# Performance work log

Hardware: AMD Instinct MI355X
Metric: run time of the kernel (lower is better)

The kernel has to match this reference:

```python
import jax, jax.numpy as jnp
import numpy as np

B, T, C = 4, 2048, 1024
H = 16
D = C // H  # 64


def setup_inputs() -> dict:
    key = jax.random.key(0)
    ks = jax.random.split(key, 3)
    scale = 1.0 / np.sqrt(C)
    return {
        "x": jax.random.normal(ks[0], (B, T, C), dtype=jnp.float32),
        "W_attn": jax.random.normal(ks[1], (C, 3 * C), dtype=jnp.float32) * scale,
        "b_attn": jnp.zeros((3 * C,), dtype=jnp.float32),
        "W_proj": jax.random.normal(ks[2], (C, C), dtype=jnp.float32) * scale,
        "b_proj": jnp.zeros((C,), dtype=jnp.float32),
    }


def reference(x, W_attn, b_attn, W_proj, b_proj):
    b, t, c = x.shape
    qkv = x @ W_attn + b_attn                      # [B,T,3C]
    q, k, v = jnp.split(qkv, 3, axis=-1)           # each [B,T,C]
    to_heads = lambda z: z.reshape(b, t, H, D).transpose(0, 2, 1, 3)  # [B,H,T,D]
    q, k, v = to_heads(q), to_heads(k), to_heads(v)
    scores = jnp.einsum("bhtd,bhsd->bhts", q, k) / jnp.sqrt(jnp.float32(D))
    causal = jnp.tril(jnp.ones((t, t), dtype=bool))  # [T,T]
    scores = jnp.where(causal[None, None], scores, jnp.finfo(scores.dtype).min)
    attn = jax.nn.softmax(scores, axis=-1)           # [B,H,T,T]
    out = jnp.einsum("bhts,bhsd->bhtd", attn, v)     # [B,H,T,D]
    out = out.transpose(0, 2, 1, 3).reshape(b, t, c)
    return out @ W_proj + b_proj
```

## Files before the change

### kernel.cpp

```cpp
#include <hip/hip_runtime.h>
#include <hip/hip_bf16.h>

typedef __bf16 bf16_t;
typedef __attribute__((ext_vector_type(8))) __bf16 bf16x8;
typedef __attribute__((ext_vector_type(4))) float f32x4;
typedef __attribute__((ext_vector_type(4))) unsigned short u16x4;

#define B_DIM 4
#define T_DIM 2048
#define C_DIM 1024
#define H_DIM 16
#define D_DIM 64
#define M_TOK (B_DIM * T_DIM)
#define N_QKV (3 * C_DIM)
#define NT    (T_DIM / 64)
#define KSTR  72
#define CSC   0.18033688011112042f

__device__ __forceinline__ void gload_lds16(const bf16_t* g, bf16_t* l) {
  __builtin_amdgcn_global_load_lds((const __attribute__((address_space(1))) void*)(g),
                                   (__attribute__((address_space(3))) void*)(l), 16, 0, 0);
}

__global__ void cvt_f32_to_bf16(const float* __restrict__ in, bf16_t* __restrict__ out, int n4) {
  int i = blockIdx.x * blockDim.x + threadIdx.x;
  if (i >= n4) return;
  float4 v = ((const float4*)in)[i];
  struct alignas(8) bv4 { bf16_t x, y, z, w; };
  bv4 o;
  o.x = (bf16_t)v.x; o.y = (bf16_t)v.y; o.z = (bf16_t)v.z; o.w = (bf16_t)v.w;
  ((bv4*)out)[i] = o;
}

__global__ void transpose_f32_to_bf16(const float* __restrict__ in, bf16_t* __restrict__ out,
                                      int K, int N) {
  __shared__ float tile[32][33];
  int bx = blockIdx.x * 32;
  int by = blockIdx.y * 32;
  int tx = threadIdx.x, ty = threadIdx.y;
#pragma unroll
  for (int i = 0; i < 32; i += 8)
    tile[ty + i][tx] = in[(size_t)(by + ty + i) * N + bx + tx];
  __syncthreads();
#pragma unroll
  for (int i = 0; i < 32; i += 8)
    out[(size_t)(bx + ty + i) * K + by + tx] = (bf16_t)tile[tx][ty + i];
}

#define BM 128
#define BN 128
#define BK 32

__global__ __launch_bounds__(256, 4)
void gemm_bt_bias(const bf16_t* __restrict__ A, const bf16_t* __restrict__ Bt,
                  const float* __restrict__ bias, bf16_t* __restrict__ Cb,
                  int M, int N, int K) {
  __shared__ alignas(16) bf16_t As[BM * BK];
  __shared__ alignas(16) bf16_t Bs[BN * BK];
  const int tid = threadIdx.x;
  const int lane = tid & 63;
  const int wave = tid >> 6;
  const int wr = (wave >> 1) * 64, wc = (wave & 1) * 64;
  const int quad = lane >> 4, l16 = lane & 15;
  const int row0 = blockIdx.x * BM, col0 = blockIdx.y * BN;

  const int srow = wave * 32 + (lane >> 2);
  const int scol = (lane & 3) * 8;
  const bf16_t* Ag = A + (size_t)(row0 + srow) * K + scol;
  const bf16_t* Bg = Bt + (size_t)(col0 + srow) * K + scol;
  bf16_t* AsW = &As[(wave * 32) * BK];
  bf16_t* BsW = &Bs[(wave * 32) * BK];

  f32x4 acc[4][4];
#pragma unroll
  for (int i = 0; i < 4; ++i)
#pragma unroll
    for (int j = 0; j < 4; ++j)
      acc[i][j] = (f32x4){0.f, 0.f, 0.f, 0.f};

  for (int k0 = 0; k0 < K; k0 += BK) {
    __syncthreads();
    gload_lds16(Ag + k0, AsW);
    gload_lds16(Ag + k0 + (size_t)16 * K, AsW + 16 * BK);
    gload_lds16(Bg + k0, BsW);
    gload_lds16(Bg + k0 + (size_t)16 * K, BsW + 16 * BK);
    __syncthreads();
    bf16x8 af[4], bfr[4];
#pragma unroll
    for (int i = 0; i < 4; ++i)
      af[i] = *(const bf16x8*)&As[(wr + i * 16 + l16) * BK + quad * 8];
#pragma unroll
    for (int j = 0; j < 4; ++j)
      bfr[j] = *(const bf16x8*)&Bs[(wc + j * 16 + l16) * BK + quad * 8];
#pragma unroll
    for (int i = 0; i < 4; ++i)
#pragma unroll
      for (int j = 0; j < 4; ++j)
        acc[i][j] = __builtin_amdgcn_mfma_f32_16x16x32_bf16(af[i], bfr[j], acc[i][j], 0, 0, 0);
  }

#pragma unroll
  for (int i = 0; i < 4; ++i)
#pragma unroll
    for (int j = 0; j < 4; ++j) {
      int col = col0 + wc + j * 16 + l16;
      float bv = bias[col];
#pragma unroll
      for (int r = 0; r < 4; ++r) {
        int row = row0 + wr + i * 16 + quad * 4 + r;
        Cb[(size_t)row * N + col] = (bf16_t)(acc[i][j][r] + bv);
      }
    }
}

__global__ __launch_bounds__(256, 4)
void gemm_bt_bias_n64(const bf16_t* __restrict__ A, const bf16_t* __restrict__ Bt,
                      const float* __restrict__ bias, float* __restrict__ Cf,
                      int M, int N, int K) {
  __shared__ alignas(16) bf16_t As[BM * BK];
  __shared__ alignas(16) bf16_t Bs[64 * BK];
  const int tid = threadIdx.x;
  const int lane = tid & 63;
  const int wave = tid >> 6;
  const int wr = (wave >> 1) * 64, wc = (wave & 1) * 32;
  const int quad = lane >> 4, l16 = lane & 15;
  const int row0 = blockIdx.x * BM, col0 = blockIdx.y * 64;

  const int sr = lane >> 2;
  const int scol = (lane & 3) * 8;
  const bf16_t* Ag = A + (size_t)(row0 + wave * 32 + sr) * K + scol;
  const bf16_t* Bg = Bt + (size_t)(col0 + wave * 16 + sr) * K + scol;
  bf16_t* AsW = &As[(wave * 32) * BK];
  bf16_t* BsW = &Bs[(wave * 16) * BK];

  f32x4 acc[4][2];
#pragma unroll
  for (int i = 0; i < 4; ++i)
#pragma unroll
    for (int j = 0; j < 2; ++j)
      acc[i][j] = (f32x4){0.f, 0.f, 0.f, 0.f};

  for (int k0 = 0; k0 < K; k0 += BK) {
    __syncthreads();
    gload_lds16(Ag + k0, AsW);
    gload_lds16(Ag + k0 + (size_t)16 * K, AsW + 16 * BK);
    gload_lds16(Bg + k0, BsW);
    __syncthreads();
    bf16x8 af[4], bfr[2];
#pragma unroll
    for (int i = 0; i < 4; ++i)
      af[i] = *(const bf16x8*)&As[(wr + i * 16 + l16) * BK + quad * 8];
#pragma unroll
    for (int j = 0; j < 2; ++j)
      bfr[j] = *(const bf16x8*)&Bs[(wc + j * 16 + l16) * BK + quad * 8];
#pragma unroll
    for (int i = 0; i < 4; ++i)
#pragma unroll
      for (int j = 0; j < 2; ++j)
        acc[i][j] = __builtin_amdgcn_mfma_f32_16x16x32_bf16(af[i], bfr[j], acc[i][j], 0, 0, 0);
  }

#pragma unroll
  for (int i = 0; i < 4; ++i)
#pragma unroll
    for (int j = 0; j < 2; ++j) {
      int col = col0 + wc + j * 16 + l16;
      float bv = bias[col];
#pragma unroll
      for (int r = 0; r < 4; ++r) {
        int row = row0 + wr + i * 16 + quad * 4 + r;
        Cf[(size_t)row * N + col] = acc[i][j][r] + bv;
      }
    }
}

__device__ __forceinline__ float exp_row_sum(f32x4 sv[4], bool diag, bf16_t* PsW,
                                             int l16, int quad, int wave) {
  if (diag) {
    const int qr = wave * 16 + l16;
#pragma unroll
    for (int ct = 0; ct < 4; ++ct)
#pragma unroll
      for (int r = 0; r < 4; ++r)
        if (ct * 16 + quad * 4 + r > qr) sv[ct][r] = -INFINITY;
  }
  float rsum = 0.f;
#pragma unroll
  for (int ct = 0; ct < 4; ++ct) {
    u16x4 pk;
#pragma unroll
    for (int r = 0; r < 4; ++r) {
      float p = __builtin_amdgcn_exp2f(sv[ct][r] * CSC);
      rsum += p;
      pk[r] = __builtin_bit_cast(unsigned short, (bf16_t)p);
    }
    *(u16x4*)&PsW[l16 * KSTR + ct * 16 + quad * 4] = pk;
  }
  rsum += __shfl_xor(rsum, 16);
  rsum += __shfl_xor(rsum, 32);
  return rsum;
}

__global__ __launch_bounds__(256, 4)
void attn_fwd(const bf16_t* __restrict__ qkv, bf16_t* __restrict__ out) {
  __shared__ alignas(16) bf16_t Ks[64 * KSTR];
  __shared__ alignas(16) bf16_t Vt[64 * KSTR];
  __shared__ alignas(16) bf16_t Ps[4 * 16 * KSTR];

  const int tid = threadIdx.x;
  const int lane = tid & 63;
  const int wave = tid >> 6;
  const int quad = lane >> 4, l16 = lane & 15;
  const int qlo = blockIdx.x;
  const int qhi = NT - 1 - qlo;
  const int h = blockIdx.y, b = blockIdx.z;
  const size_t tokBase = (size_t)b * T_DIM;

  const bf16_t* qpl = qkv + (tokBase + qlo * 64 + wave * 16 + l16) * N_QKV + h * D_DIM;
  const bf16_t* qph = qkv + (tokBase + qhi * 64 + wave * 16 + l16) * N_QKV + h * D_DIM;
  bf16x8 ql0 = *(const bf16x8*)(qpl + quad * 8);
  bf16x8 ql1 = *(const bf16x8*)(qpl + 32 + quad * 8);
  bf16x8 qh0 = *(const bf16x8*)(qph + quad * 8);
  bf16x8 qh1 = *(const bf16x8*)(qph + 32 + quad * 8);

  f32x4 ol[4], oh[4];
#pragma unroll
  for (int dt = 0; dt < 4; ++dt) {
    ol[dt] = (f32x4){0.f, 0.f, 0.f, 0.f};
    oh[dt] = (f32x4){0.f, 0.f, 0.f, 0.f};
  }
  float ll = 0.f, lh = 0.f;

  const int tx = tid & 15, ty = tid >> 4;
  bf16_t* PsW = &Ps[wave * 16 * KSTR];
  const f32x4 zero4 = (f32x4){0.f, 0.f, 0.f, 0.f};

  u16x4 kreg[4], vreg[4];
  const bf16_t* kb0 = qkv + (tokBase + ty * 4) * N_QKV + h * D_DIM + C_DIM + tx * 4;
#pragma unroll
  for (int r = 0; r < 4; ++r) kreg[r] = *(const u16x4*)(kb0 + (size_t)r * N_QKV);
#pragma unroll
  for (int r = 0; r < 4; ++r) vreg[r] = *(const u16x4*)(kb0 + (size_t)r * N_QKV + C_DIM);

  for (int t = 0; t <= qhi; ++t) {
    const bool lo = (t <= qlo);
    __syncthreads();
#pragma unroll
    for (int r = 0; r < 4; ++r)
      *(u16x4*)&Ks[(ty * 4 + r) * KSTR + tx * 4] = kreg[r];
#pragma unroll
    for (int i = 0; i < 4; ++i) {
      u16x4 p = (u16x4){vreg[0][i], vreg[1][i], vreg[2][i], vreg[3][i]};
      *(u16x4*)&Vt[(tx * 4 + i) * KSTR + ty * 4] = p;
    }
    __syncthreads();
    if (t < qhi) {
      const bf16_t* kb = qkv + (tokBase + (t + 1) * 64 + ty * 4) * N_QKV + h * D_DIM + C_DIM + tx * 4;
#pragma unroll
      for (int r = 0; r < 4; ++r) kreg[r] = *(const u16x4*)(kb + (size_t)r * N_QKV);
#pragma unroll
      for (int r = 0; r < 4; ++r) vreg[r] = *(const u16x4*)(kb + (size_t)r * N_QKV + C_DIM);
    }

    f32x4 svl[4], svh[4];
#pragma unroll
    for (int ct = 0; ct < 4; ++ct) {
      bf16x8 kf0 = *(const bf16x8*)&Ks[(ct * 16 + l16) * KSTR + quad * 8];
      bf16x8 kf1 = *(const bf16x8*)&Ks[(ct * 16 + l16) * KSTR + 32 + quad * 8];
      if (lo) {
        svl[ct] = __builtin_amdgcn_mfma_f32_16x16x32_bf16(kf0, ql0, zero4, 0, 0, 0);
        svl[ct] = __builtin_amdgcn_mfma_f32_16x16x32_bf16(kf1, ql1, svl[ct], 0, 0, 0);
      }
      svh[ct] = __builtin_amdgcn_mfma_f32_16x16x32_bf16(kf0, qh0, zero4, 0, 0, 0);
      svh[ct] = __builtin_amdgcn_mfma_f32_16x16x32_bf16(kf1, qh1, svh[ct], 0, 0, 0);
    }

    bf16x8 pl0, pl1, ph0, ph1;
    if (lo) {
      ll += exp_row_sum(svl, t == qlo, PsW, l16, quad, wave);
      pl0 = *(const bf16x8*)&PsW[l16 * KSTR + quad * 8];
      pl1 = *(const bf16x8*)&PsW[l16 * KSTR + 32 + quad * 8];
    }
    lh += exp_row_sum(svh, t == qhi, PsW, l16, quad, wave);
    ph0 = *(const bf16x8*)&PsW[l16 * KSTR + quad * 8];
    ph1 = *(const bf16x8*)&PsW[l16 * KSTR + 32 + quad * 8];

#pragma unroll
    for (int dt = 0; dt < 4; ++dt) {
      bf16x8 vf0 = *(const bf16x8*)&Vt[(dt * 16 + l16) * KSTR + quad * 8];
      bf16x8 vf1 = *(const bf16x8*)&Vt[(dt * 16 + l16) * KSTR + 32 + quad * 8];
      if (lo) {
        ol[dt] = __builtin_amdgcn_mfma_f32_16x16x32_bf16(vf0, pl0, ol[dt], 0, 0, 0);
        ol[dt] = __builtin_amdgcn_mfma_f32_16x16x32_bf16(vf1, pl1, ol[dt], 0, 0, 0);
      }
      oh[dt] = __builtin_amdgcn_mfma_f32_16x16x32_bf16(vf0, ph0, oh[dt], 0, 0, 0);
      oh[dt] = __builtin_amdgcn_mfma_f32_16x16x32_bf16(vf1, ph1, oh[dt], 0, 0, 0);
    }
  }

  struct alignas(8) bh4 { bf16_t a, b, c, d; };
  {
    float rl = 1.0f / ll;
    bf16_t* op = out + (tokBase + qlo * 64 + wave * 16 + l16) * C_DIM + h * D_DIM;
#pragma unroll
    for (int dt = 0; dt < 4; ++dt) {
      bh4 v = {(bf16_t)(ol[dt][0] * rl), (bf16_t)(ol[dt][1] * rl),
               (bf16_t)(ol[dt][2] * rl), (bf16_t)(ol[dt][3] * rl)};
      *(bh4*)(op + dt * 16 + quad * 4) = v;
    }
  }
  {
    float rl = 1.0f / lh;
    bf16_t* op = out + (tokBase + qhi * 64 + wave * 16 + l16) * C_DIM + h * D_DIM;
#pragma unroll
    for (int dt = 0; dt < 4; ++dt) {
      bh4 v = {(bf16_t)(oh[dt][0] * rl), (bf16_t)(oh[dt][1] * rl),
               (bf16_t)(oh[dt][2] * rl), (bf16_t)(oh[dt][3] * rl)};
      *(bh4*)(op + dt * 16 + quad * 4) = v;
    }
  }
}

extern "C" void kernel_launch(void* const* d_in, const int* in_sizes, int n_in,
                              void* d_out, int out_size, void* d_ws, size_t ws_size,
                              hipStream_t stream) {
  const float* x      = (const float*)d_in[0];
  const float* W_attn = (const float*)d_in[1];
  const float* b_attn = (const float*)d_in[2];
  const float* W_proj = (const float*)d_in[3];
  const float* b_proj = (const float*)d_in[4];
  float* out = (float*)d_out;

  char* ws = (char*)d_ws;
  bf16_t* xb   = (bf16_t*)ws;  ws += (size_t)M_TOK * C_DIM * 2;
  bf16_t* Wat  = (bf16_t*)ws;  ws += (size_t)N_QKV * C_DIM * 2;
  bf16_t* Wpt  = (bf16_t*)ws;  ws += (size_t)C_DIM * C_DIM * 2;
  bf16_t* qkv  = (bf16_t*)ws;  ws += (size_t)M_TOK * N_QKV * 2;
  bf16_t* attn = (bf16_t*)ws;  ws += (size_t)M_TOK * C_DIM * 2;

  {
    int n4 = (M_TOK * C_DIM) / 4;
    cvt_f32_to_bf16<<<n4 / 256, 256, 0, stream>>>(x, xb, n4);
  }
  transpose_f32_to_bf16<<<dim3(N_QKV / 32, C_DIM / 32), dim3(32, 8), 0, stream>>>(W_attn, Wat, C_DIM, N_QKV);
  transpose_f32_to_bf16<<<dim3(C_DIM / 32, C_DIM / 32), dim3(32, 8), 0, stream>>>(W_proj, Wpt, C_DIM, C_DIM);

  gemm_bt_bias<<<dim3(M_TOK / BM, N_QKV / BN), 256, 0, stream>>>(
      xb, Wat, b_attn, qkv, M_TOK, N_QKV, C_DIM);

  attn_fwd<<<dim3(NT / 2, H_DIM, B_DIM), 256, 0, stream>>>(qkv, attn);

  gemm_bt_bias_n64<<<dim3(M_TOK / BM, C_DIM / 64), 256, 0, stream>>>(
      attn, Wpt, b_proj, out, M_TOK, C_DIM, C_DIM);
}
```

Before: 280.8 us.

## Replace paired lo/hi query-tile attention blocks with one tile per block

The attention kernel no longer pairs a short causal tile with a long one in each block for load balance. Each block now handles a single 64-row query tile, the grid doubles, and blocks are ordered longest-first so heavy tiles start early. Each K/V tile loaded into LDS now feeds only one query tile instead of two, but each block needs fewer registers and a block's work ends at its own diagonal. Packed-integer types are also swapped for bf16 vector types, which is cosmetic.

```diff
diff --git a/kernel.cpp b/kernel.cpp
--- a/kernel.cpp
+++ b/kernel.cpp
@@ -2,9 +2,9 @@
 #include <hip/hip_bf16.h>
 
 typedef __bf16 bf16_t;
+typedef __attribute__((ext_vector_type(4))) __bf16 bf16x4;
 typedef __attribute__((ext_vector_type(8))) __bf16 bf16x8;
 typedef __attribute__((ext_vector_type(4))) float f32x4;
-typedef __attribute__((ext_vector_type(4))) unsigned short u16x4;
 
 #define B_DIM 4
 #define T_DIM 2048
@@ -26,10 +26,9 @@
   int i = blockIdx.x * blockDim.x + threadIdx.x;
   if (i >= n4) return;
   float4 v = ((const float4*)in)[i];
-  struct alignas(8) bv4 { bf16_t x, y, z, w; };
-  bv4 o;
-  o.x = (bf16_t)v.x; o.y = (bf16_t)v.y; o.z = (bf16_t)v.z; o.w = (bf16_t)v.w;
-  ((bv4*)out)[i] = o;
+  bf16x4 o;
+  o[0] = (bf16_t)v.x; o[1] = (bf16_t)v.y; o[2] = (bf16_t)v.z; o[3] = (bf16_t)v.w;
+  ((bf16x4*)out)[i] = o;
 }
 
 __global__ void transpose_f32_to_bf16(const float* __restrict__ in, bf16_t* __restrict__ out,
@@ -187,14 +186,14 @@
   float rsum = 0.f;
 #pragma unroll
   for (int ct = 0; ct < 4; ++ct) {
-    u16x4 pk;
+    bf16x4 pk;
 #pragma unroll
     for (int r = 0; r < 4; ++r) {
       float p = __builtin_amdgcn_exp2f(sv[ct][r] * CSC);
       rsum += p;
-      pk[r] = __builtin_bit_cast(unsigned short, (bf16_t)p);
-    }
-    *(u16x4*)&PsW[l16 * KSTR + ct * 16 + quad * 4] = pk;
+      pk[r] = (bf16_t)p;
+    }
+    *(bf16x4*)&PsW[l16 * KSTR + ct * 16 + quad * 4] = pk;
   }
   rsum += __shfl_xor(rsum, 16);
   rsum += __shfl_xor(rsum, 32);
@@ -211,113 +210,80 @@
   const int lane = tid & 63;
   const int wave = tid >> 6;
   const int quad = lane >> 4, l16 = lane & 15;
-  const int qlo = blockIdx.x;
-  const int qhi = NT - 1 - qlo;
+  const int qt = NT - 1 - blockIdx.x;
   const int h = blockIdx.y, b = blockIdx.z;
   const size_t tokBase = (size_t)b * T_DIM;
 
-  const bf16_t* qpl = qkv + (tokBase + qlo * 64 + wave * 16 + l16) * N_QKV + h * D_DIM;
-  const bf16_t* qph = qkv + (tokBase + qhi * 64 + wave * 16 + l16) * N_QKV + h * D_DIM;
-  bf16x8 ql0 = *(const bf16x8*)(qpl + quad * 8);
-  bf16x8 ql1 = *(const bf16x8*)(qpl + 32 + quad * 8);
-  bf16x8 qh0 = *(const bf16x8*)(qph + quad * 8);
-  bf16x8 qh1 = *(const bf16x8*)(qph + 32 + quad * 8);
-
-  f32x4 ol[4], oh[4];
-#pragma unroll
-  for (int dt = 0; dt < 4; ++dt) {
-    ol[dt] = (f32x4){0.f, 0.f, 0.f, 0.f};
-    oh[dt] = (f32x4){0.f, 0.f, 0.f, 0.f};
-  }
-  float ll = 0.f, lh = 0.f;
+  const bf16_t* qp = qkv + (tokBase + qt * 64 + wave * 16 + l16) * N_QKV + h * D_DIM;
+  bf16x8 q0 = *(const bf16x8*)(qp + quad * 8);
+  bf16x8 q1 = *(const bf16x8*)(qp + 32 + quad * 8);
+
+  f32x4 o_acc[4];
+#pragma unroll
+  for (int dt = 0; dt < 4; ++dt) o_acc[dt] = (f32x4){0.f, 0.f, 0.f, 0.f};
+  float lsum = 0.f;
 
   const int tx = tid & 15, ty = tid >> 4;
   bf16_t* PsW = &Ps[wave * 16 * KSTR];
   const f32x4 zero4 = (f32x4){0.f, 0.f, 0.f, 0.f};
 
-  u16x4 kreg[4], vreg[4];
+  bf16x4 kreg[4], vreg[4];
   const bf16_t* kb0 = qkv + (tokBase + ty * 4) * N_QKV + h * D_DIM + C_DIM + tx * 4;
 #pragma unroll
-  for (int r = 0; r < 4; ++r) kreg[r] = *(const u16x4*)(kb0 + (size_t)r * N_QKV);
-#pragma unroll
-  for (int r = 0; r < 4; ++r) vreg[r] = *(const u16x4*)(kb0 + (size_t)r * N_QKV + C_DIM);
-
-  for (int t = 0; t <= qhi; ++t) {
-    const bool lo = (t <= qlo);
+  for (int r = 0; r < 4; ++r) kreg[r] = *(const bf16x4*)(kb0 + (size_t)r * N_QKV);
+#pragma unroll
+  for (int r = 0; r < 4; ++r) vreg[r] = *(const bf16x4*)(kb0 + (size_t)r * N_QKV + C_DIM);
+
+  for (int t = 0; t <= qt; ++t) {
     __syncthreads();
 #pragma unroll
     for (int r = 0; r < 4; ++r)
-      *(u16x4*)&Ks[(ty * 4 + r) * KSTR + tx * 4] = kreg[r];
+      *(bf16x4*)&Ks[(ty * 4 + r) * KSTR + tx * 4] = kreg[r];
 #pragma unroll
     for (int i = 0; i < 4; ++i) {
-      u16x4 p = (u16x4){vreg[0][i], vreg[1][i], vreg[2][i], vreg[3][i]};
-      *(u16x4*)&Vt[(tx * 4 + i) * KSTR + ty * 4] = p;
-    }
-    __syncthreads();
-    if (t < qhi) {
+      bf16x4 p;
+      p[0] = vreg[0][i]; p[1] = vreg[1][i]; p[2] = vreg[2][i]; p[3] = vreg[3][i];
+      *(bf16x4*)&Vt[(tx * 4 + i) * KSTR + ty * 4] = p;
+    }
+    __syncthreads();
+    if (t < qt) {
       const bf16_t* kb = qkv + (tokBase + (t + 1) * 64 + ty * 4) * N_QKV + h * D_DIM + C_DIM + tx * 4;
 #pragma unroll
-      for (int r = 0; r < 4; ++r) kreg[r] = *(const u16x4*)(kb + (size_t)r * N_QKV);
-#pragma unroll
-      for (int r = 0; r < 4; ++r) vreg[r] = *(const u16x4*)(kb + (size_t)r * N_QKV + C_DIM);
-    }
-
-    f32x4 svl[4], svh[4];
+      for (int r = 0; r < 4; ++r) kreg[r] = *(const bf16x4*)(kb + (size_t)r * N_QKV);
+#pragma unroll
+      for (int r = 0; r < 4; ++r) vreg[r] = *(const bf16x4*)(kb + (size_t)r * N_QKV + C_DIM);
+    }
+
+    f32x4 sv[4];
 #pragma unroll
     for (int ct = 0; ct < 4; ++ct) {
       bf16x8 kf0 = *(const bf16x8*)&Ks[(ct * 16 + l16) * KSTR + quad * 8];
       bf16x8 kf1 = *(const bf16x8*)&Ks[(ct * 16 + l16) * KSTR + 32 + quad * 8];
-      if (lo) {
-        svl[ct] = __builtin_amdgcn_mfma_f32_16x16x32_bf16(kf0, ql0, zero4, 0, 0, 0);
-        svl[ct] = __builtin_amdgcn_mfma_f32_16x16x32_bf16(kf1, ql1, svl[ct], 0, 0, 0);
-      }
-      svh[ct] = __builtin_amdgcn_mfma_f32_16x16x32_bf16(kf0, qh0, zero4, 0, 0, 0);
-      svh[ct] = __builtin_amdgcn_mfma_f32_16x16x32_bf16(kf1, qh1, svh[ct], 0, 0, 0);
-    }
-
-    bf16x8 pl0, pl1, ph0, ph1;
-    if (lo) {
-      ll += exp_row_sum(svl, t == qlo, PsW, l16, quad, wave);
-      pl0 = *(const bf16x8*)&PsW[l16 * KSTR + quad * 8];
-      pl1 = *(const bf16x8*)&PsW[l16 * KSTR + 32 + quad * 8];
-    }
-    lh += exp_row_sum(svh, t == qhi, PsW, l16, quad, wave);
-    ph0 = *(const bf16x8*)&PsW[l16 * KSTR + quad * 8];
-    ph1 = *(const bf16x8*)&PsW[l16 * KSTR + 32 + quad * 8];
+      sv[ct] = __builtin_amdgcn_mfma_f32_16x16x32_bf16(kf0, q0, zero4, 0, 0, 0);
+      sv[ct] = __builtin_amdgcn_mfma_f32_16x16x32_bf16(kf1, q1, sv[ct], 0, 0, 0);
+    }
+
+    lsum += exp_row_sum(sv, t == qt, PsW, l16, quad, wave);
+    bf16x8 p0 = *(const bf16x8*)&PsW[l16 * KSTR + quad * 8];
+    bf16x8 p1 = *(const bf16x8*)&PsW[l16 * KSTR + 32 + quad * 8];
 
 #pragma unroll
     for (int dt = 0; dt < 4; ++dt) {
       bf16x8 vf0 = *(const bf16x8*)&Vt[(dt * 16 + l16) * KSTR + quad * 8];
       bf16x8 vf1 = *(const bf16x8*)&Vt[(dt * 16 + l16) * KSTR + 32 + quad * 8];
-      if (lo) {
-        ol[dt] = __builtin_amdgcn_mfma_f32_16x16x32_bf16(vf0, pl0, ol[dt], 0, 0, 0);
-        ol[dt] = __builtin_amdgcn_mfma_f32_16x16x32_bf16(vf1, pl1, ol[dt], 0, 0, 0);
-      }
-      oh[dt] = __builtin_amdgcn_mfma_f32_16x16x32_bf16(vf0, ph0, oh[dt], 0, 0, 0);
-      oh[dt] = __builtin_amdgcn_mfma_f32_16x16x32_bf16(vf1, ph1, oh[dt], 0, 0, 0);
-    }
-  }
-
-  struct alignas(8) bh4 { bf16_t a, b, c, d; };
-  {
-    float rl = 1.0f / ll;
-    bf16_t* op = out + (tokBase + qlo * 64 + wave * 16 + l16) * C_DIM + h * D_DIM;
-#pragma unroll
-    for (int dt = 0; dt < 4; ++dt) {
-      bh4 v = {(bf16_t)(ol[dt][0] * rl), (bf16_t)(ol[dt][1] * rl),
-               (bf16_t)(ol[dt][2] * rl), (bf16_t)(ol[dt][3] * rl)};
-      *(bh4*)(op + dt * 16 + quad * 4) = v;
-    }
-  }
-  {
-    float rl = 1.0f / lh;
-    bf16_t* op = out + (tokBase + qhi * 64 + wave * 16 + l16) * C_DIM + h * D_DIM;
-#pragma unroll
-    for (int dt = 0; dt < 4; ++dt) {
-      bh4 v = {(bf16_t)(oh[dt][0] * rl), (bf16_t)(oh[dt][1] * rl),
-               (bf16_t)(oh[dt][2] * rl), (bf16_t)(oh[dt][3] * rl)};
-      *(bh4*)(op + dt * 16 + quad * 4) = v;
-    }
+      o_acc[dt] = __builtin_amdgcn_mfma_f32_16x16x32_bf16(vf0, p0, o_acc[dt], 0, 0, 0);
+      o_acc[dt] = __builtin_amdgcn_mfma_f32_16x16x32_bf16(vf1, p1, o_acc[dt], 0, 0, 0);
+    }
+  }
+
+  float rl = 1.0f / lsum;
+  bf16_t* op = out + (tokBase + qt * 64 + wave * 16 + l16) * C_DIM + h * D_DIM;
+#pragma unroll
+  for (int dt = 0; dt < 4; ++dt) {
+    bf16x4 v;
+    v[0] = (bf16_t)(o_acc[dt][0] * rl); v[1] = (bf16_t)(o_acc[dt][1] * rl);
+    v[2] = (bf16_t)(o_acc[dt][2] * rl); v[3] = (bf16_t)(o_acc[dt][3] * rl);
+    *(bf16x4*)(op + dt * 16 + quad * 4) = v;
   }
 }
 
@@ -348,7 +314,7 @@
   gemm_bt_bias<<<dim3(M_TOK / BM, N_QKV / BN), 256, 0, stream>>>(
       xb, Wat, b_attn, qkv, M_TOK, N_QKV, C_DIM);
 
-  attn_fwd<<<dim3(NT / 2, H_DIM, B_DIM), 256, 0, stream>>>(qkv, attn);
+  attn_fwd<<<dim3(NT, H_DIM, B_DIM), 256, 0, stream>>>(qkv, attn);
 
   gemm_bt_bias_n64<<<dim3(M_TOK / BM, C_DIM / 64), 256, 0, stream>>>(
       attn, Wpt, b_proj, out, M_TOK, C_DIM, C_DIM);
```

After: 345.7 us. 1.23x slower.
